# Optimization experiments

Measured on AMD Instinct MI355X. Metric: run time of the kernel, lower is better.

The kernel has to match this reference:

```python
import jax, jax.numpy as jnp
import numpy as np

N = 50000      # nodes
E = 800000     # edges (avg degree 16)
DIN = 128
DOUT = 64
ALPHA = 0.5    # DirGATConv mixing coefficient
NEG_SLOPE = 0.2  # PyG GATConv default negative_slope


def setup_inputs() -> dict:
    key = jax.random.key(0)
    ks = jax.random.split(key, 12)
    x = jax.random.normal(ks[0], (N, DIN), jnp.float32)
    edge_index = jax.random.randint(ks[1], (2, E), 0, N, dtype=jnp.int64)

    def p(k, shape):
        return jax.random.normal(k, shape, jnp.float32) * 0.05

    return dict(
        x=x,
        edge_index=edge_index,
        W1=p(ks[2], (DIN, DOUT)), att_src1=p(ks[3], (DOUT,)), att_dst1=p(ks[4], (DOUT,)), b1=jnp.zeros((DOUT,), jnp.float32),
        W2=p(ks[5], (DIN, DOUT)), att_src2=p(ks[6], (DOUT,)), att_dst2=p(ks[7], (DOUT,)), b2=jnp.zeros((DOUT,), jnp.float32),
    )


def _gat_conv(x, src, dst, W, a_src, a_dst, b):
    """PyG GATConv with heads=1: linear, per-dst softmax attention, scatter-add."""
    n = x.shape[0]
    loops = jnp.arange(n, dtype=src.dtype)
    src = jnp.concatenate([src, loops])  # add_self_loops=True (PyG default)
    dst = jnp.concatenate([dst, loops])

    xw = x @ W                                # [N, DOUT]
    a_s = xw @ a_src                          # [N]  per-node src attention score
    a_d = xw @ a_dst                          # [N]  per-node dst attention score
    e = jax.nn.leaky_relu(a_s[src] + a_d[dst], NEG_SLOPE)  # [E+N]

    # numerically-stable softmax over edges grouped by destination node
    m = jax.ops.segment_max(e, dst, num_segments=n)
    m = jnp.where(jnp.isfinite(m), m, 0.0)    # nodes w/o in-edges -> safe value
    ex = jnp.exp(e - m[dst])
    denom = jax.ops.segment_sum(ex, dst, num_segments=n)
    coef = ex / (denom[dst] + 1e-16)          # [E+N]

    out = jax.ops.segment_sum(coef[:, None] * xw[src], dst, num_segments=n)
    return out + b


def reference(x, edge_index, W1, att_src1, att_dst1, b1, W2, att_src2, att_dst2, b2):
    src, dst = edge_index[0], edge_index[1]
    out_fwd = _gat_conv(x, src, dst, W1, att_src1, att_dst1, b1)   # src -> dst
    out_rev = _gat_conv(x, dst, src, W2, att_src2, att_dst2, b2)   # dst -> src (transposed edges)
    return (1.0 - ALPHA) * out_fwd + ALPHA * out_rev
```

## Files before the change

### kernel.cpp

```cpp
#include <hip/hip_runtime.h>

#define DIN 128
#define DOUT 64
#define NEG_SLOPE 0.2f
#define ALPHA 0.5f
#define NBUK 512
#define EPB  4096
#define BCCAP 6144

typedef __attribute__((ext_vector_type(8))) short bf16x8;
typedef __attribute__((ext_vector_type(4))) float f32x4;

__device__ __forceinline__ float lrelu(float x) { return x > 0.0f ? x : NEG_SLOPE * x; }

__device__ __forceinline__ unsigned short f2bf(float f) {
    unsigned u = __float_as_uint(f);
    unsigned r = (u + 0x7fffu + ((u >> 16) & 1u)) >> 16;
    return (unsigned short)r;
}
__device__ __forceinline__ float bf2f(unsigned short h) {
    return __uint_as_float((unsigned)h << 16);
}
__device__ __forceinline__ float readlane_f(float v, int l) {
    return __int_as_float(__builtin_amdgcn_readlane(__float_as_int(v), l));
}


__device__ __forceinline__ void dev_wfrag(
    const float* __restrict__ W1, const float* __restrict__ W2,
    unsigned short* __restrict__ wf, int blk, int tid)
{
    int combo = blk * 4 + (tid >> 6);
    int mat = combo >> 4;
    int kk = (combo >> 2) & 3;
    int t = combo & 3;
    int l = tid & 63;
    int g = l >> 4, c = l & 15;
    const float* W = mat ? W2 : W1;
    #pragma unroll
    for (int j = 0; j < 8; ++j) {
        float w = W[(kk * 32 + g * 8 + j) * DOUT + t * 16 + c];
        unsigned short hi = f2bf(w);
        unsigned short lo = f2bf(w - bf2f(hi));
        wf[(size_t)(((mat * 2 + 0) * 16 + kk * 4 + t) * 512) + l * 8 + j] = hi;
        wf[(size_t)(((mat * 2 + 1) * 16 + kk * 4 + t) * 512) + l * 8 + j] = lo;
    }
}

__device__ __forceinline__ void dev_binhist(
    const int* __restrict__ src, const int* __restrict__ dst,
    int* __restrict__ hist, int e, int n, int nblk, int blk, int tid, int* cnt)
{
    for (int b = tid; b < NBUK; b += 256) cnt[b] = 0;
    __syncthreads();
    int base = blk * EPB;
    for (int k = 0; k < EPB / 256; ++k) {
        int t = base + k * 256 + tid;
        if (t < e) {
            int s = src[t], d = dst[t];
            atomicAdd(&cnt[d >> 8], 1);
            atomicAdd(&cnt[(n + s) >> 8], 1);
        }
    }
    __syncthreads();
    for (int b = tid; b < NBUK; b += 256)
        hist[(size_t)b * nblk + blk] = cnt[b];
}

__device__ __forceinline__ void dev_scan_part(
    const int* __restrict__ deg, int* __restrict__ part, int L, int blk, int tid, int* sm)
{
    int base = blk * 1024 + tid * 4;
    int s = 0;
    #pragma unroll
    for (int k = 0; k < 4; ++k) { int i = base + k; if (i < L) s += deg[i]; }
    sm[tid] = s; __syncthreads();
    for (int o = 128; o; o >>= 1) { if (tid < o) sm[tid] += sm[tid + o]; __syncthreads(); }
    if (tid == 0) part[blk] = sm[0];
}

__device__ __forceinline__ void dev_scan_mid(
    int* __restrict__ part, int nb, int* __restrict__ hscan, int L, int total,
    int tid, int* sm)
{
    int v = (tid < nb) ? part[tid] : 0;
    sm[tid] = v; __syncthreads();
    for (int o = 1; o < 256; o <<= 1) {
        int u = (tid >= o) ? sm[tid - o] : 0;
        __syncthreads();
        sm[tid] += u;
        __syncthreads();
    }
    if (tid < nb) part[tid] = sm[tid] - v;
    if (tid == 0) hscan[L] = total;
}

__device__ __forceinline__ void dev_scan_apply(
    const int* __restrict__ deg, const int* __restrict__ part,
    int* __restrict__ hscan, int L, int blk, int tid, int* sm)
{
    int base = blk * 1024 + tid * 4;
    int d[4]; int s = 0;
    #pragma unroll
    for (int k = 0; k < 4; ++k) { int i = base + k; d[k] = (i < L) ? deg[i] : 0; s += d[k]; }
    sm[tid] = s; __syncthreads();
    for (int o = 1; o < 256; o <<= 1) {
        int u = (tid >= o) ? sm[tid - o] : 0;
        __syncthreads();
        sm[tid] += u;
        __syncthreads();
    }
    int run = part[blk] + sm[tid] - s;
    #pragma unroll
    for (int k = 0; k < 4; ++k) {
        int i = base + k;
        if (i < L) { hscan[i] = run; run += d[k]; }
    }
}

__device__ __forceinline__ void dev_binscatter(
    const int* __restrict__ src, const int* __restrict__ dst,
    const int* __restrict__ hscan, unsigned* __restrict__ staging,
    int e, int n, int nblk, int blk, int tid, int* cur)
{
    for (int b = tid; b < NBUK; b += 256)
        cur[b] = hscan[(size_t)b * nblk + blk];
    __syncthreads();
    int base = blk * EPB;
    for (int k = 0; k < EPB / 256; ++k) {
        int t = base + k * 256 + tid;
        if (t < e) {
            int s = src[t], d = dst[t];
            int pF = atomicAdd(&cur[d >> 8], 1);
            staging[pF] = ((unsigned)(d & 255) << 16) | (unsigned)s;
            int segR = n + s;
            int pR = atomicAdd(&cur[segR >> 8], 1);
            staging[pR] = ((unsigned)(segR & 255) << 16) | (unsigned)d;
        }
    }
}

__device__ __forceinline__ void dev_proj(
    const float* __restrict__ x, const unsigned short* __restrict__ wf,
    const float* __restrict__ as1, const float* __restrict__ ad1,
    const float* __restrict__ as2, const float* __restrict__ ad2,
    unsigned short* __restrict__ xw1, unsigned short* __restrict__ xw2,
    float* __restrict__ s1, float* __restrict__ d1,
    float* __restrict__ s2, float* __restrict__ d2, int n, int projblk, int tid)
{
    int ntiles = (n + 15) >> 4;
    int tile = projblk * 4 + (tid >> 6);
    if (tile >= ntiles) return;
    int l = tid & 63;
    int g = l >> 4, c = l & 15;

    int arow = tile * 16 + c;
    if (arow >= n) arow = n - 1;

    bf16x8 ahi[4], alo[4];
    const float* xr = x + (size_t)arow * DIN + g * 8;
    #pragma unroll
    for (int kk = 0; kk < 4; ++kk) {
        float4 v0 = *(const float4*)(xr + kk * 32);
        float4 v1 = *(const float4*)(xr + kk * 32 + 4);
        float xv[8] = {v0.x, v0.y, v0.z, v0.w, v1.x, v1.y, v1.z, v1.w};
        #pragma unroll
        for (int j = 0; j < 8; ++j) {
            unsigned short hi = f2bf(xv[j]);
            unsigned short lo = f2bf(xv[j] - bf2f(hi));
            ahi[kk][j] = (short)hi;
            alo[kk][j] = (short)lo;
        }
    }

    float vs1[4] = {0, 0, 0, 0}, vd1[4] = {0, 0, 0, 0};
    float vs2[4] = {0, 0, 0, 0}, vd2[4] = {0, 0, 0, 0};
    const bf16x8* wfv = (const bf16x8*)wf;

    #pragma unroll
    for (int t = 0; t < 4; ++t) {
        f32x4 C1 = {0.f, 0.f, 0.f, 0.f}, C2 = {0.f, 0.f, 0.f, 0.f};
        #pragma unroll
        for (int kk = 0; kk < 4; ++kk) {
            bf16x8 bh1 = wfv[(size_t)((0 * 16 + kk * 4 + t) * 64) + l];
            bf16x8 bl1 = wfv[(size_t)((1 * 16 + kk * 4 + t) * 64) + l];
            bf16x8 bh2 = wfv[(size_t)((2 * 16 + kk * 4 + t) * 64) + l];
            bf16x8 bl2 = wfv[(size_t)((3 * 16 + kk * 4 + t) * 64) + l];
            C1 = __builtin_amdgcn_mfma_f32_16x16x32_bf16(ahi[kk], bh1, C1, 0, 0, 0);
            C1 = __builtin_amdgcn_mfma_f32_16x16x32_bf16(alo[kk], bh1, C1, 0, 0, 0);
            C1 = __builtin_amdgcn_mfma_f32_16x16x32_bf16(ahi[kk], bl1, C1, 0, 0, 0);
            C2 = __builtin_amdgcn_mfma_f32_16x16x32_bf16(ahi[kk], bh2, C2, 0, 0, 0);
            C2 = __builtin_amdgcn_mfma_f32_16x16x32_bf16(alo[kk], bh2, C2, 0, 0, 0);
            C2 = __builtin_amdgcn_mfma_f32_16x16x32_bf16(ahi[kk], bl2, C2, 0, 0, 0);
        }
        float a1v = as1[t * 16 + c], a2v = ad1[t * 16 + c];
        float a3v = as2[t * 16 + c], a4v = ad2[t * 16 + c];
        #pragma unroll
        for (int r = 0; r < 4; ++r) {
            vs1[r] = fmaf(C1[r], a1v, vs1[r]);
            vd1[r] = fmaf(C1[r], a2v, vd1[r]);
            vs2[r] = fmaf(C2[r], a3v, vs2[r]);
            vd2[r] = fmaf(C2[r], a4v, vd2[r]);
        }
        #pragma unroll
        for (int r = 0; r < 4; ++r) {
            int node = tile * 16 + g * 4 + r;
            if (node < n) {
                xw1[(size_t)node * DOUT + t * 16 + c] = f2bf(C1[r]);
                xw2[(size_t)node * DOUT + t * 16 + c] = f2bf(C2[r]);
            }
        }
    }
    #pragma unroll
    for (int off = 1; off < 16; off <<= 1) {
        #pragma unroll
        for (int r = 0; r < 4; ++r) {
            vs1[r] += __shfl_xor(vs1[r], off);
            vd1[r] += __shfl_xor(vd1[r], off);
            vs2[r] += __shfl_xor(vs2[r], off);
            vd2[r] += __shfl_xor(vd2[r], off);
        }
    }
    if (c == 0) {
        #pragma unroll
        for (int r = 0; r < 4; ++r) {
            int node = tile * 16 + g * 4 + r;
            if (node < n) {
                s1[node] = vs1[r]; d1[node] = vd1[r];
                s2[node] = vs2[r]; d2[node] = vd2[r];
            }
        }
    }
}


__global__ __launch_bounds__(256) void fused1_kernel(
    const float* __restrict__ W1, const float* __restrict__ W2,
    unsigned short* __restrict__ wf,
    const int* __restrict__ src, const int* __restrict__ dst,
    int* __restrict__ hist, int e, int n, int nblk)
{
    __shared__ int smem[NBUK];
    int blk = blockIdx.x, tid = threadIdx.x;
    if (blk < 8) dev_wfrag(W1, W2, wf, blk, tid);
    else dev_binhist(src, dst, hist, e, n, nblk, blk - 8, tid, smem);
}

__global__ __launch_bounds__(256) void fused2_kernel(
    const int* __restrict__ hist, int* __restrict__ part, int L, int ntile,
    const float* __restrict__ x, const unsigned short* __restrict__ wf,
    const float* __restrict__ as1, const float* __restrict__ ad1,
    const float* __restrict__ as2, const float* __restrict__ ad2,
    unsigned short* __restrict__ xw1, unsigned short* __restrict__ xw2,
    float* __restrict__ s1, float* __restrict__ d1,
    float* __restrict__ s2, float* __restrict__ d2, int n, int proj0)
{
    __shared__ int smem[256];
    int blk = blockIdx.x, tid = threadIdx.x;
    if (blk < ntile) dev_scan_part(hist, part, L, blk, tid, smem);
    else dev_proj(x, wf, as1, ad1, as2, ad2, xw1, xw2, s1, d1, s2, d2, n,
                  proj0 + blk - ntile, tid);
}

__global__ __launch_bounds__(256) void fused3_kernel(
    int* __restrict__ part, int ntile, int* __restrict__ hscan, int L, int total,
    const float* __restrict__ x, const unsigned short* __restrict__ wf,
    const float* __restrict__ as1, const float* __restrict__ ad1,
    const float* __restrict__ as2, const float* __restrict__ ad2,
    unsigned short* __restrict__ xw1, unsigned short* __restrict__ xw2,
    float* __restrict__ s1, float* __restrict__ d1,
    float* __restrict__ s2, float* __restrict__ d2, int n, int proj0)
{
    __shared__ int smem[256];
    int blk = blockIdx.x, tid = threadIdx.x;
    if (blk == 0) dev_scan_mid(part, ntile, hscan, L, total, tid, smem);
    else dev_proj(x, wf, as1, ad1, as2, ad2, xw1, xw2, s1, d1, s2, d2, n,
                  proj0 + blk - 1, tid);
}

__global__ __launch_bounds__(256) void fused4_kernel(
    const int* __restrict__ hist, const int* __restrict__ part,
    int* __restrict__ hscan, int L, int ntile,
    const float* __restrict__ x, const unsigned short* __restrict__ wf,
    const float* __restrict__ as1, const float* __restrict__ ad1,
    const float* __restrict__ as2, const float* __restrict__ ad2,
    unsigned short* __restrict__ xw1, unsigned short* __restrict__ xw2,
    float* __restrict__ s1, float* __restrict__ d1,
    float* __restrict__ s2, float* __restrict__ d2, int n, int proj0)
{
    __shared__ int smem[256];
    int blk = blockIdx.x, tid = threadIdx.x;
    if (blk < ntile) dev_scan_apply(hist, part, hscan, L, blk, tid, smem);
    else dev_proj(x, wf, as1, ad1, as2, ad2, xw1, xw2, s1, d1, s2, d2, n,
                  proj0 + blk - ntile, tid);
}

__global__ __launch_bounds__(256) void fused5_kernel(
    const int* __restrict__ src, const int* __restrict__ dst,
    const int* __restrict__ hscan, unsigned* __restrict__ staging,
    int e, int nblk,
    const float* __restrict__ x, const unsigned short* __restrict__ wf,
    const float* __restrict__ as1, const float* __restrict__ ad1,
    const float* __restrict__ as2, const float* __restrict__ ad2,
    unsigned short* __restrict__ xw1, unsigned short* __restrict__ xw2,
    float* __restrict__ s1, float* __restrict__ d1,
    float* __restrict__ s2, float* __restrict__ d2, int n, int proj0)
{
    __shared__ int smem[NBUK];
    int blk = blockIdx.x, tid = threadIdx.x;
    if (blk < nblk) dev_binscatter(src, dst, hscan, staging, e, n, nblk, blk, tid, smem);
    else dev_proj(x, wf, as1, ad1, as2, ad2, xw1, xw2, s1, d1, s2, d2, n,
                  proj0 + blk - nblk, tid);
}

__global__ __launch_bounds__(256) void buildcsr_kernel(
    const int* __restrict__ hscan, const unsigned* __restrict__ staging,
    int* __restrict__ csr, int* __restrict__ offs,
    int n2, int e2, int nblk)
{
    __shared__ int segcnt[256];
    __shared__ int segoff[256];
    __shared__ unsigned cache[BCCAP];
    int b = blockIdx.x, tid = threadIdx.x;
    int lo = hscan[(size_t)b * nblk];
    int hi = hscan[(size_t)(b + 1) * nblk];
    int span = hi - lo;
    segcnt[tid] = 0;
    __syncthreads();
    if (span <= BCCAP) {
        for (int k = tid; k < span; k += 256) {
            unsigned st = staging[lo + k];
            cache[k] = st;
            atomicAdd(&segcnt[st >> 16], 1);
        }
    } else {
        for (int idx = lo + tid; idx < hi; idx += 256)
            atomicAdd(&segcnt[staging[idx] >> 16], 1);
    }
    __syncthreads();
    if (tid < 64) {
        int a0 = segcnt[4 * tid], a1 = segcnt[4 * tid + 1];
        int a2 = segcnt[4 * tid + 2], a3 = segcnt[4 * tid + 3];
        int s = a0 + a1 + a2 + a3;
        int inc = s;
        #pragma unroll
        for (int off = 1; off < 64; off <<= 1) {
            int u = __shfl_up(inc, off);
            if (tid >= off) inc += u;
        }
        int excl = inc - s;
        segoff[4 * tid] = excl;
        segoff[4 * tid + 1] = excl + a0;
        segoff[4 * tid + 2] = excl + a0 + a1;
        segoff[4 * tid + 3] = excl + a0 + a1 + a2;
    }
    __syncthreads();
    {
        int seg = (b << 8) + tid;
        if (seg < n2) offs[seg] = lo + segoff[tid];
        segcnt[tid] = segoff[tid];
    }
    if (b == gridDim.x - 1 && tid == 0) offs[n2] = e2;
    __syncthreads();
    if (span <= BCCAP) {
        for (int k = tid; k < span; k += 256) {
            unsigned st = cache[k];
            int pos = atomicAdd(&segcnt[st >> 16], 1);
            csr[lo + pos] = (int)(st & 0xFFFFu);
        }
    } else {
        for (int idx = lo + tid; idx < hi; idx += 256) {
            unsigned st = staging[idx];
            int pos = atomicAdd(&segcnt[st >> 16], 1);
            csr[lo + pos] = (int)(st & 0xFFFFu);
        }
    }
}

__global__ __launch_bounds__(256) void gather_kernel(
    const int* __restrict__ offs, const int* __restrict__ csr,
    const float* __restrict__ s1, const float* __restrict__ d1,
    const float* __restrict__ s2, const float* __restrict__ d2,
    const unsigned short* __restrict__ xw1, const unsigned short* __restrict__ xw2,
    const float* __restrict__ b1, const float* __restrict__ b2,
    float* __restrict__ out, int n)
{
    int i = (blockIdx.x * 256 + threadIdx.x) >> 6;
    int lane = threadIdx.x & 63;
    if (i >= n) return;

    float d1i = d1[i], d2i = d2[i];
    int cF = offs[i],     endF = offs[i + 1];
    int cR = offs[n + i], endR = offs[n + i + 1];

    float pSF = __expf(lrelu(s1[i] + d1i));
    float pSR = __expf(lrelu(s2[i] + d2i));
    float lF = pSF, lR = pSR;
    float aF0 = pSF * bf2f(xw1[(size_t)i * DOUT + lane]), aF1 = 0.f, aF2 = 0.f, aF3 = 0.f;
    float aR0 = pSR * bf2f(xw2[(size_t)i * DOUT + lane]), aR1 = 0.f, aR2 = 0.f, aR3 = 0.f;

    while (cF < endF || cR < endR) {
        int cntF = endF - cF; cntF = cntF < 0 ? 0 : (cntF > 64 ? 64 : cntF);
        int cntR = endR - cR; cntR = cntR < 0 ? 0 : (cntR > 64 ? 64 : cntR);

        int jF = 0, jR = 0;
        float pF = 0.0f, pR = 0.0f;
        if (lane < cntF) { jF = csr[cF + lane]; pF = __expf(lrelu(s1[jF] + d1i)); }
        if (lane < cntR) { jR = csr[cR + lane]; pR = __expf(lrelu(s2[jR] + d2i)); }

        float psF = pF, psR = pR;
        #pragma unroll
        for (int off = 32; off; off >>= 1) {
            psF += __shfl_xor(psF, off);
            psR += __shfl_xor(psR, off);
        }
        lF += psF;
        lR += psR;

        int tmax = cntF > cntR ? cntF : cntR;
        int t = 0;
        for (; t + 4 <= tmax; t += 4) {
            float pF0 = readlane_f(pF, t),     pF1 = readlane_f(pF, t + 1);
            float pF2 = readlane_f(pF, t + 2), pF3 = readlane_f(pF, t + 3);
            int   jF0 = __builtin_amdgcn_readlane(jF, t);
            int   jF1 = __builtin_amdgcn_readlane(jF, t + 1);
            int   jF2 = __builtin_amdgcn_readlane(jF, t + 2);
            int   jF3 = __builtin_amdgcn_readlane(jF, t + 3);
            float pR0 = readlane_f(pR, t),     pR1 = readlane_f(pR, t + 1);
            float pR2 = readlane_f(pR, t + 2), pR3 = readlane_f(pR, t + 3);
            int   jR0 = __builtin_amdgcn_readlane(jR, t);
            int   jR1 = __builtin_amdgcn_readlane(jR, t + 1);
            int   jR2 = __builtin_amdgcn_readlane(jR, t + 2);
            int   jR3 = __builtin_amdgcn_readlane(jR, t + 3);
            aF0 = fmaf(pF0, bf2f(xw1[(size_t)jF0 * DOUT + lane]), aF0);
            aF1 = fmaf(pF1, bf2f(xw1[(size_t)jF1 * DOUT + lane]), aF1);
            aF2 = fmaf(pF2, bf2f(xw1[(size_t)jF2 * DOUT + lane]), aF2);
            aF3 = fmaf(pF3, bf2f(xw1[(size_t)jF3 * DOUT + lane]), aF3);
            aR0 = fmaf(pR0, bf2f(xw2[(size_t)jR0 * DOUT + lane]), aR0);
            aR1 = fmaf(pR1, bf2f(xw2[(size_t)jR1 * DOUT + lane]), aR1);
            aR2 = fmaf(pR2, bf2f(xw2[(size_t)jR2 * DOUT + lane]), aR2);
            aR3 = fmaf(pR3, bf2f(xw2[(size_t)jR3 * DOUT + lane]), aR3);
        }
        for (; t < tmax; ++t) {
            float pF0 = readlane_f(pF, t);
            int   jF0 = __builtin_amdgcn_readlane(jF, t);
            float pR0 = readlane_f(pR, t);
            int   jR0 = __builtin_amdgcn_readlane(jR, t);
            aF0 = fmaf(pF0, bf2f(xw1[(size_t)jF0 * DOUT + lane]), aF0);
            aR0 = fmaf(pR0, bf2f(xw2[(size_t)jR0 * DOUT + lane]), aR0);
        }
        cF += cntF;
        cR += cntR;
    }

    float resF = ((aF0 + aF1) + (aF2 + aF3)) / (lF + 1e-16f);
    float resR = ((aR0 + aR1) + (aR2 + aR3)) / (lR + 1e-16f);
    out[(size_t)i * DOUT + lane] =
        (1.0f - ALPHA) * (resF + b1[lane]) + ALPHA * (resR + b2[lane]);
}

extern "C" void kernel_launch(void* const* d_in, const int* in_sizes, int n_in,
                              void* d_out, int out_size, void* d_ws, size_t ws_size,
                              hipStream_t stream) {
    const float* x   = (const float*)d_in[0];
    const int*   ei  = (const int*)d_in[1];
    const float* W1  = (const float*)d_in[2];
    const float* as1 = (const float*)d_in[3];
    const float* ad1 = (const float*)d_in[4];
    const float* b1  = (const float*)d_in[5];
    const float* W2  = (const float*)d_in[6];
    const float* as2 = (const float*)d_in[7];
    const float* ad2 = (const float*)d_in[8];
    const float* b2  = (const float*)d_in[9];
    float* out = (float*)d_out;

    int n = in_sizes[0] / DIN;
    int e = in_sizes[1] / 2;
    const int* src = ei;
    const int* dst = ei + e;
    int n2 = 2 * n;
    int e2 = 2 * e;
    int nblk = (e + EPB - 1) / EPB;
    int L = NBUK * nblk;
    int ntile = (L + 1023) / 1024;
    int nbuk_eff = (n2 + 255) >> 8;
    int ntiles16 = (n + 15) >> 4;
    int projblks = (ntiles16 + 3) / 4;

    int pc0 = projblks / 4, pc1 = projblks / 4, pc2 = projblks / 4;
    int pc3 = projblks - pc0 - pc1 - pc2;

    unsigned short* xw1 = (unsigned short*)d_ws;
    unsigned short* xw2 = xw1 + (size_t)n * DOUT;
    float* s1  = (float*)(xw2 + (size_t)n * DOUT);
    float* d1  = s1 + n;
    float* s2  = d1 + n;
    float* d2  = s2 + n;
    unsigned short* wf = (unsigned short*)(d2 + n);
    int* hist  = (int*)(wf + 32768);
    int* hscan = hist + (size_t)L;
    int* part  = hscan + (size_t)L + 1;
    int* offs  = part + 1024;
    int* csr   = offs + (size_t)n2 + 1;
    unsigned* staging = (unsigned*)(csr + (size_t)e2);

    fused1_kernel<<<8 + nblk, 256, 0, stream>>>(W1, W2, wf, src, dst, hist, e, n, nblk);

    fused2_kernel<<<ntile + pc0, 256, 0, stream>>>(hist, part, L, ntile,
        x, wf, as1, ad1, as2, ad2, xw1, xw2, s1, d1, s2, d2, n, 0);

    fused3_kernel<<<1 + pc1, 256, 0, stream>>>(part, ntile, hscan, L, e2,
        x, wf, as1, ad1, as2, ad2, xw1, xw2, s1, d1, s2, d2, n, pc0);

    fused4_kernel<<<ntile + pc2, 256, 0, stream>>>(hist, part, hscan, L, ntile,
        x, wf, as1, ad1, as2, ad2, xw1, xw2, s1, d1, s2, d2, n, pc0 + pc1);

    fused5_kernel<<<nblk + pc3, 256, 0, stream>>>(src, dst, hscan, staging, e, nblk,
        x, wf, as1, ad1, as2, ad2, xw1, xw2, s1, d1, s2, d2, n, pc0 + pc1 + pc2);

    buildcsr_kernel<<<nbuk_eff, 256, 0, stream>>>(hscan, staging, csr, offs, n2, e2, nblk);

    long long gthreads = (long long)n * 64;
    int gblocks = (int)((gthreads + 255) / 256);
    gather_kernel<<<gblocks, 256, 0, stream>>>(offs, csr, s1, d1, s2, d2,
                                               xw1, xw2, b1, b2, out, n);
}
```

Baseline: 113.1 us.

## Drop split-bf16 projection, process two tiles per wave, accumulate softmax denom via readlane

```diff
diff --git a/kernel.cpp b/kernel.cpp
--- a/kernel.cpp
+++ b/kernel.cpp
@@ -40,10 +40,7 @@
     #pragma unroll
     for (int j = 0; j < 8; ++j) {
         float w = W[(kk * 32 + g * 8 + j) * DOUT + t * 16 + c];
-        unsigned short hi = f2bf(w);
-        unsigned short lo = f2bf(w - bf2f(hi));
-        wf[(size_t)(((mat * 2 + 0) * 16 + kk * 4 + t) * 512) + l * 8 + j] = hi;
-        wf[(size_t)(((mat * 2 + 1) * 16 + kk * 4 + t) * 512) + l * 8 + j] = lo;
+        wf[(size_t)((mat * 16 + kk * 4 + t) * 512) + l * 8 + j] = f2bf(w);
     }
 }
 
@@ -149,85 +146,85 @@
     float* __restrict__ s2, float* __restrict__ d2, int n, int projblk, int tid)
 {
     int ntiles = (n + 15) >> 4;
-    int tile = projblk * 4 + (tid >> 6);
-    if (tile >= ntiles) return;
+    int tbase = projblk * 8 + (tid >> 6) * 2;
+    if (tbase >= ntiles) return;
     int l = tid & 63;
     int g = l >> 4, c = l & 15;
 
-    int arow = tile * 16 + c;
-    if (arow >= n) arow = n - 1;
-
-    bf16x8 ahi[4], alo[4];
-    const float* xr = x + (size_t)arow * DIN + g * 8;
-    #pragma unroll
-    for (int kk = 0; kk < 4; ++kk) {
-        float4 v0 = *(const float4*)(xr + kk * 32);
-        float4 v1 = *(const float4*)(xr + kk * 32 + 4);
-        float xv[8] = {v0.x, v0.y, v0.z, v0.w, v1.x, v1.y, v1.z, v1.w};
+    bf16x8 ah[2][4];
+    #pragma unroll
+    for (int u = 0; u < 2; ++u) {
+        int arow = (tbase + u) * 16 + c;
+        if (arow >= n) arow = n - 1;
+        const float* xr = x + (size_t)arow * DIN + g * 8;
         #pragma unroll
-        for (int j = 0; j < 8; ++j) {
-            unsigned short hi = f2bf(xv[j]);
-            unsigned short lo = f2bf(xv[j] - bf2f(hi));
-            ahi[kk][j] = (short)hi;
-            alo[kk][j] = (short)lo;
-        }
-    }
-
-    float vs1[4] = {0, 0, 0, 0}, vd1[4] = {0, 0, 0, 0};
-    float vs2[4] = {0, 0, 0, 0}, vd2[4] = {0, 0, 0, 0};
+        for (int kk = 0; kk < 4; ++kk) {
+            float4 v0 = *(const float4*)(xr + kk * 32);
+            float4 v1 = *(const float4*)(xr + kk * 32 + 4);
+            float xv[8] = {v0.x, v0.y, v0.z, v0.w, v1.x, v1.y, v1.z, v1.w};
+            #pragma unroll
+            for (int j = 0; j < 8; ++j) ah[u][kk][j] = (short)f2bf(xv[j]);
+        }
+    }
+
+    float vs1[2][4] = {}, vd1[2][4] = {}, vs2[2][4] = {}, vd2[2][4] = {};
     const bf16x8* wfv = (const bf16x8*)wf;
 
     #pragma unroll
     for (int t = 0; t < 4; ++t) {
-        f32x4 C1 = {0.f, 0.f, 0.f, 0.f}, C2 = {0.f, 0.f, 0.f, 0.f};
+        f32x4 C1[2] = {{0.f,0.f,0.f,0.f},{0.f,0.f,0.f,0.f}};
+        f32x4 C2[2] = {{0.f,0.f,0.f,0.f},{0.f,0.f,0.f,0.f}};
         #pragma unroll
         for (int kk = 0; kk < 4; ++kk) {
             bf16x8 bh1 = wfv[(size_t)((0 * 16 + kk * 4 + t) * 64) + l];
-            bf16x8 bl1 = wfv[(size_t)((1 * 16 + kk * 4 + t) * 64) + l];
-            bf16x8 bh2 = wfv[(size_t)((2 * 16 + kk * 4 + t) * 64) + l];
-            bf16x8 bl2 = wfv[(size_t)((3 * 16 + kk * 4 + t) * 64) + l];
-            C1 = __builtin_amdgcn_mfma_f32_16x16x32_bf16(ahi[kk], bh1, C1, 0, 0, 0);
-            C1 = __builtin_amdgcn_mfma_f32_16x16x32_bf16(alo[kk], bh1, C1, 0, 0, 0);
-            C1 = __builtin_amdgcn_mfma_f32_16x16x32_bf16(ahi[kk], bl1, C1, 0, 0, 0);
-            C2 = __builtin_amdgcn_mfma_f32_16x16x32_bf16(ahi[kk], bh2, C2, 0, 0, 0);
-            C2 = __builtin_amdgcn_mfma_f32_16x16x32_bf16(alo[kk], bh2, C2, 0, 0, 0);
-            C2 = __builtin_amdgcn_mfma_f32_16x16x32_bf16(ahi[kk], bl2, C2, 0, 0, 0);
+            bf16x8 bh2 = wfv[(size_t)((1 * 16 + kk * 4 + t) * 64) + l];
+            #pragma unroll
+            for (int u = 0; u < 2; ++u) {
+                C1[u] = __builtin_amdgcn_mfma_f32_16x16x32_bf16(ah[u][kk], bh1, C1[u], 0, 0, 0);
+                C2[u] = __builtin_amdgcn_mfma_f32_16x16x32_bf16(ah[u][kk], bh2, C2[u], 0, 0, 0);
+            }
         }
         float a1v = as1[t * 16 + c], a2v = ad1[t * 16 + c];
         float a3v = as2[t * 16 + c], a4v = ad2[t * 16 + c];
         #pragma unroll
-        for (int r = 0; r < 4; ++r) {
-            vs1[r] = fmaf(C1[r], a1v, vs1[r]);
-            vd1[r] = fmaf(C1[r], a2v, vd1[r]);
-            vs2[r] = fmaf(C2[r], a3v, vs2[r]);
-            vd2[r] = fmaf(C2[r], a4v, vd2[r]);
-        }
-        #pragma unroll
-        for (int r = 0; r < 4; ++r) {
-            int node = tile * 16 + g * 4 + r;
-            if (node < n) {
-                xw1[(size_t)node * DOUT + t * 16 + c] = f2bf(C1[r]);
-                xw2[(size_t)node * DOUT + t * 16 + c] = f2bf(C2[r]);
+        for (int u = 0; u < 2; ++u) {
+            #pragma unroll
+            for (int r = 0; r < 4; ++r) {
+                vs1[u][r] = fmaf(C1[u][r], a1v, vs1[u][r]);
+                vd1[u][r] = fmaf(C1[u][r], a2v, vd1[u][r]);
+                vs2[u][r] = fmaf(C2[u][r], a3v, vs2[u][r]);
+                vd2[u][r] = fmaf(C2[u][r], a4v, vd2[u][r]);
+                int node = (tbase + u) * 16 + g * 4 + r;
+                if (node < n) {
+                    xw1[(size_t)node * DOUT + t * 16 + c] = f2bf(C1[u][r]);
+                    xw2[(size_t)node * DOUT + t * 16 + c] = f2bf(C2[u][r]);
+                }
             }
         }
     }
     #pragma unroll
     for (int off = 1; off < 16; off <<= 1) {
         #pragma unroll
-        for (int r = 0; r < 4; ++r) {
-            vs1[r] += __shfl_xor(vs1[r], off);
-            vd1[r] += __shfl_xor(vd1[r], off);
-            vs2[r] += __shfl_xor(vs2[r], off);
-            vd2[r] += __shfl_xor(vd2[r], off);
+        for (int u = 0; u < 2; ++u) {
+            #pragma unroll
+            for (int r = 0; r < 4; ++r) {
+                vs1[u][r] += __shfl_xor(vs1[u][r], off);
+                vd1[u][r] += __shfl_xor(vd1[u][r], off);
+                vs2[u][r] += __shfl_xor(vs2[u][r], off);
+                vd2[u][r] += __shfl_xor(vd2[u][r], off);
+            }
         }
     }
     if (c == 0) {
         #pragma unroll
-        for (int r = 0; r < 4; ++r) {
-            int node = tile * 16 + g * 4 + r;
-            if (node < n) {
-                s1[node] = vs1[r]; d1[node] = vd1[r];
-                s2[node] = vs2[r]; d2[node] = vd2[r];
+        for (int u = 0; u < 2; ++u) {
+            #pragma unroll
+            for (int r = 0; r < 4; ++r) {
+                int node = (tbase + u) * 16 + g * 4 + r;
+                if (node < n) {
+                    s1[node] = vs1[u][r]; d1[node] = vd1[u][r];
+                    s2[node] = vs2[u][r]; d2[node] = vd2[u][r];
+                }
             }
         }
     }
@@ -395,7 +392,7 @@
 
     float pSF = __expf(lrelu(s1[i] + d1i));
     float pSR = __expf(lrelu(s2[i] + d2i));
-    float lF = pSF, lR = pSR;
+    float lF0 = pSF, lF1 = 0.f, lR0 = pSR, lR1 = 0.f;
     float aF0 = pSF * bf2f(xw1[(size_t)i * DOUT + lane]), aF1 = 0.f, aF2 = 0.f, aF3 = 0.f;
     float aR0 = pSR * bf2f(xw2[(size_t)i * DOUT + lane]), aR1 = 0.f, aR2 = 0.f, aR3 = 0.f;
 
@@ -407,15 +404,6 @@
         float pF = 0.0f, pR = 0.0f;
         if (lane < cntF) { jF = csr[cF + lane]; pF = __expf(lrelu(s1[jF] + d1i)); }
         if (lane < cntR) { jR = csr[cR + lane]; pR = __expf(lrelu(s2[jR] + d2i)); }
-
-        float psF = pF, psR = pR;
-        #pragma unroll
-        for (int off = 32; off; off >>= 1) {
-            psF += __shfl_xor(psF, off);
-            psR += __shfl_xor(psR, off);
-        }
-        lF += psF;
-        lR += psR;
 
         int tmax = cntF > cntR ? cntF : cntR;
         int t = 0;
@@ -432,6 +420,8 @@
             int   jR1 = __builtin_amdgcn_readlane(jR, t + 1);
             int   jR2 = __builtin_amdgcn_readlane(jR, t + 2);
             int   jR3 = __builtin_amdgcn_readlane(jR, t + 3);
+            lF0 += pF0 + pF1; lF1 += pF2 + pF3;
+            lR0 += pR0 + pR1; lR1 += pR2 + pR3;
             aF0 = fmaf(pF0, bf2f(xw1[(size_t)jF0 * DOUT + lane]), aF0);
             aF1 = fmaf(pF1, bf2f(xw1[(size_t)jF1 * DOUT + lane]), aF1);
             aF2 = fmaf(pF2, bf2f(xw1[(size_t)jF2 * DOUT + lane]), aF2);
@@ -446,6 +436,7 @@
             int   jF0 = __builtin_amdgcn_readlane(jF, t);
             float pR0 = readlane_f(pR, t);
             int   jR0 = __builtin_amdgcn_readlane(jR, t);
+            lF0 += pF0; lR0 += pR0;
             aF0 = fmaf(pF0, bf2f(xw1[(size_t)jF0 * DOUT + lane]), aF0);
             aR0 = fmaf(pR0, bf2f(xw2[(size_t)jR0 * DOUT + lane]), aR0);
         }
@@ -453,6 +444,7 @@
         cR += cntR;
     }
 
+    float lF = lF0 + lF1, lR = lR0 + lR1;
     float resF = ((aF0 + aF1) + (aF2 + aF3)) / (lF + 1e-16f);
     float resR = ((aR0 + aR1) + (aR2 + aR3)) / (lR + 1e-16f);
     out[(size_t)i * DOUT + lane] =
@@ -485,7 +477,7 @@
     int ntile = (L + 1023) / 1024;
     int nbuk_eff = (n2 + 255) >> 8;
     int ntiles16 = (n + 15) >> 4;
-    int projblks = (ntiles16 + 3) / 4;
+    int projblks = (ntiles16 + 7) / 8;
 
     int pc0 = projblks / 4, pc1 = projblks / 4, pc2 = projblks / 4;
     int pc3 = projblks - pc0 - pc1 - pc2;
@@ -497,7 +489,7 @@
     float* s2  = d1 + n;
     float* d2  = s2 + n;
     unsigned short* wf = (unsigned short*)(d2 + n);
-    int* hist  = (int*)(wf + 32768);
+    int* hist  = (int*)(wf + 16384);
     int* hscan = hist + (size_t)L;
     int* part  = hscan + (size_t)L + 1;
     int* offs  = part + 1024;
```

Measured after the change: 115.2 us. No clear change (+1.9%).
